# Kernel tuning notes

Measured on AMD Instinct MI355X. Metric: run time of the kernel, lower is better.

Reference implementation:

```python
import jax, jax.numpy as jnp
import numpy as np

N, M, D = 32768, 4096, 128  # samples, SOM units (64x64), input_dim
GRID_H, GRID_W = 64, 64


def setup_inputs() -> dict:
    key = jax.random.key(0)
    k1, k2 = jax.random.split(key)
    inputs = jax.random.normal(k1, (N, D), dtype=jnp.float32)
    # SOM2D.__init__: weights = torch.rand(size, input_dim)
    weights = jax.random.uniform(k2, (M, D), dtype=jnp.float32)
    # grid = meshgrid(arange(H), arange(W)) -> [M, 2] integer unit coordinates
    gx, gy = jnp.meshgrid(jnp.arange(GRID_H), jnp.arange(GRID_W), indexing='ij')
    grid = jnp.stack([gx, gy], axis=-1).reshape(-1, 2).astype(jnp.int32)
    return {"inputs": inputs, "weights": weights, "grid": grid}


def reference(inputs, weights, grid):
    # sed(x, y): squared Euclidean distance [N, M].
    # tensor the torch code materializes; same math.
    x_sq = jnp.sum(inputs * inputs, axis=1, keepdims=True)        # [N, 1]
    w_sq = jnp.sum(weights * weights, axis=1)                      # [M]
    cross = jnp.einsum('nd,md->nm', inputs, weights)               # [N, M]
    distances = x_sq + w_sq - 2.0 * cross                          # [N, M]
    # wtac: argmin over units, then lookup grid coordinates of the winner.
    winning_indices = jnp.argmin(distances, axis=1)                # [N]
    winning_labels = grid[winning_indices]                         # [N, 2]
    return winning_labels
```

## Files before the change

### kernel.cpp

```cpp
#include <hip/hip_runtime.h>
#include <float.h>
#include <stdint.h>


constexpr int D = 128;

typedef _Float16 f16x8 __attribute__((ext_vector_type(8)));
typedef float    f32x4 __attribute__((ext_vector_type(4)));

__device__ __forceinline__ void cvt_split(const float4& a0, const float4& a1,
                                          f16x8& h, f16x8& l) {
    float v[8] = {a0.x, a0.y, a0.z, a0.w, a1.x, a1.y, a1.z, a1.w};
#pragma unroll
    for (int j = 0; j < 8; ++j) {
        _Float16 hh = (_Float16)v[j];
        h[j] = hh;
        l[j] = (_Float16)(v[j] - (float)hh);
    }
}

__global__ __launch_bounds__(256) void prep_kernel(
        const float* __restrict__ w, f16x8* __restrict__ hG,
        f16x8* __restrict__ lG, float* __restrict__ wsq, int M) {
    int g = blockIdx.x * 256 + threadIdx.x;
    if (g >= M * 16) return;
    int u = g >> 4, o = g & 15;
    const float4* wp = reinterpret_cast<const float4*>(w + (size_t)u * D + o * 8);
    float4 a0 = wp[0], a1 = wp[1];
    f16x8 h, l;
    cvt_split(a0, a1, h, l);
    float ss = 0.f;
    ss = fmaf(a0.x, a0.x, ss); ss = fmaf(a0.y, a0.y, ss);
    ss = fmaf(a0.z, a0.z, ss); ss = fmaf(a0.w, a0.w, ss);
    ss = fmaf(a1.x, a1.x, ss); ss = fmaf(a1.y, a1.y, ss);
    ss = fmaf(a1.z, a1.z, ss); ss = fmaf(a1.w, a1.w, ss);
#pragma unroll
    for (int m = 1; m < 16; m <<= 1) ss += __shfl_xor(ss, m, 64);
    if (o == 0) wsq[u] = ss;
    int slot = ((u >> 5) << 9) + ((o >> 2) << 7) + (((u >> 4) & 1) << 6)
             + ((o & 3) << 4) + (u & 15);
    hG[slot] = h;
    lG[slot] = l;
}

__global__ void finalize(const unsigned long long* __restrict__ keys,
                         const int* __restrict__ grid, int* __restrict__ out,
                         int N, int UG) {
    int s = blockIdx.x * blockDim.x + threadIdx.x;
    if (s >= N) return;
    unsigned long long k = keys[s];
    for (int g = 1; g < UG; ++g) {
        unsigned long long kg = keys[(size_t)g * N + s];
        if (kg < k) k = kg;
    }
    int idx = (int)(unsigned)(k & 0xFFFFFFFFull);
    out[2 * s]     = grid[2 * idx];
    out[2 * s + 1] = grid[2 * idx + 1];
}

template <bool PARTIAL>
__global__ __launch_bounds__(256, 2) void som_main(
        const float* __restrict__ x, const f16x8* __restrict__ hG,
        const f16x8* __restrict__ lG, const float* __restrict__ wsq,
        const int* __restrict__ grid, int* __restrict__ out,
        unsigned long long* __restrict__ keys,
        int unitGroups, int M, int N) {
    __shared__ f16x8 albuf[4 * 1024];

    const int tid  = threadIdx.x;
    const int lane = tid & 63;
    const int wv   = tid >> 6;
    const int c    = lane & 15;
    const int q    = lane >> 4;

    const int ug    = blockIdx.x % unitGroups;
    const int sg    = blockIdx.x / unitGroups;
    const int sWave = sg * 256 + wv * 64;

    f16x8* myAl = &albuf[wv * 1024];

    f16x8 Ah[16];
#pragma unroll
    for (int i = 0; i < 4; ++i) {
        const float* xr = x + (size_t)(sWave + 16 * i + c) * D + q * 8;
#pragma unroll
        for (int s = 0; s < 4; ++s) {
            float4 a0 = *reinterpret_cast<const float4*>(xr + 32 * s);
            float4 a1 = *reinterpret_cast<const float4*>(xr + 32 * s + 4);
            f16x8 h, l;
            cvt_split(a0, a1, h, l);
            Ah[i * 4 + s] = h;
            myAl[(i * 4 + s) * 64 + lane] = l;
        }
    }

    float bestD[16];
    int   bestI[16];
#pragma unroll
    for (int sl = 0; sl < 16; ++sl) { bestD[sl] = FLT_MAX; bestI[sl] = 0; }

    const int tilesPer = (M / 32) / unitGroups;
    const int tile0    = ug * tilesPer;

    for (int tt = 0; tt < tilesPer; ++tt) {
        const int tile = tile0 + tt;
        const f16x8* hp = hG + ((size_t)tile << 9) + lane;
        const f16x8* lp = lG + ((size_t)tile << 9) + lane;

        f16x8 bh[8], bl[8];
#pragma unroll
        for (int s = 0; s < 4; ++s)
#pragma unroll
            for (int t = 0; t < 2; ++t)
                bh[s * 2 + t] = hp[s * 128 + t * 64];
#pragma unroll
        for (int s = 0; s < 4; ++s)
#pragma unroll
            for (int t = 0; t < 2; ++t)
                bl[s * 2 + t] = lp[s * 128 + t * 64];

        const int uTile = tile * 32;
        const float wq0 = wsq[uTile + c];
        const float wq1 = wsq[uTile + 16 + c];

        f32x4 acc[8];
#pragma unroll
        for (int f = 0; f < 8; ++f) acc[f] = (f32x4){0.f, 0.f, 0.f, 0.f};

#pragma unroll
        for (int s = 0; s < 4; ++s)
#pragma unroll
            for (int i = 0; i < 4; ++i)
#pragma unroll
                for (int t = 0; t < 2; ++t)
                    acc[i * 2 + t] = __builtin_amdgcn_mfma_f32_16x16x32_f16(
                        Ah[i * 4 + s], bh[s * 2 + t], acc[i * 2 + t], 0, 0, 0);
#pragma unroll
        for (int s = 0; s < 4; ++s) {
            f16x8 al[4];
#pragma unroll
            for (int i = 0; i < 4; ++i) al[i] = myAl[(i * 4 + s) * 64 + lane];
#pragma unroll
            for (int i = 0; i < 4; ++i)
#pragma unroll
                for (int t = 0; t < 2; ++t)
                    acc[i * 2 + t] = __builtin_amdgcn_mfma_f32_16x16x32_f16(
                        al[i], bh[s * 2 + t], acc[i * 2 + t], 0, 0, 0);
        }
#pragma unroll
        for (int s = 0; s < 4; ++s)
#pragma unroll
            for (int i = 0; i < 4; ++i)
#pragma unroll
                for (int t = 0; t < 2; ++t)
                    acc[i * 2 + t] = __builtin_amdgcn_mfma_f32_16x16x32_f16(
                        Ah[i * 4 + s], bl[s * 2 + t], acc[i * 2 + t], 0, 0, 0);

#pragma unroll
        for (int t = 0; t < 2; ++t) {
            const int n    = uTile + 16 * t + c;
            const float wq = t == 0 ? wq0 : wq1;
#pragma unroll
            for (int i = 0; i < 4; ++i) {
                f32x4 a = acc[i * 2 + t];
#pragma unroll
                for (int r = 0; r < 4; ++r) {
                    float score = fmaf(-2.f, a[r], wq);
                    int sl = i * 4 + r;
                    if (score < bestD[sl]) { bestD[sl] = score; bestI[sl] = n; }
                }
            }
        }
    }

#pragma unroll
    for (int sl = 0; sl < 16; ++sl) {
        float d   = bestD[sl];
        int   idx = bestI[sl];
#pragma unroll
        for (int m = 1; m < 16; m <<= 1) {
            float od = __shfl_xor(d, m, 64);
            int   oi = __shfl_xor(idx, m, 64);
            if (od < d || (od == d && oi < idx)) { d = od; idx = oi; }
        }
        if (c == 0) {
            const int sOut = sWave + 16 * (sl >> 2) + 4 * q + (sl & 3);
            if (PARTIAL) {
                unsigned ub = __float_as_uint(d);
                ub = (ub & 0x80000000u) ? ~ub : (ub | 0x80000000u);
                unsigned long long key = ((unsigned long long)ub << 32) | (unsigned)idx;
                keys[(size_t)ug * N + sOut] = key;
            } else {
                out[2 * sOut]     = grid[2 * idx];
                out[2 * sOut + 1] = grid[2 * idx + 1];
            }
        }
    }
}

extern "C" void kernel_launch(void* const* d_in, const int* in_sizes, int n_in,
                              void* d_out, int out_size, void* d_ws, size_t ws_size,
                              hipStream_t stream) {
    const float* x    = (const float*)d_in[0];
    const float* w    = (const float*)d_in[1];
    const int*   grid = (const int*)d_in[2];
    int* out = (int*)d_out;

    const int N = in_sizes[0] / D;
    const int M = in_sizes[1] / D;

    const size_t hlBytes   = (size_t)M * D * 2;
    const size_t baseBytes = 2 * hlBytes + (size_t)M * 4;

    f16x8* hG  = (f16x8*)d_ws;
    f16x8* lG  = (f16x8*)((char*)d_ws + hlBytes);
    float* wsq = (float*)((char*)d_ws + 2 * hlBytes);
    unsigned long long* keys = (unsigned long long*)((char*)d_ws + baseBytes);

    prep_kernel<<<(M * 16 + 255) / 256, 256, 0, stream>>>(w, hG, lG, wsq, M);

    const int sampleGroups = N / 256;
    int UG = 0;
    if (ws_size >= baseBytes + 4ull * N * 8) UG = 4;
    else if (ws_size >= baseBytes + 2ull * N * 8) UG = 2;

    if (UG > 0) {
        som_main<true><<<sampleGroups * UG, 256, 0, stream>>>(
            x, hG, lG, wsq, grid, out, keys, UG, M, N);
        finalize<<<(N + 255) / 256, 256, 0, stream>>>(keys, grid, out, N, UG);
    } else {
        som_main<false><<<sampleGroups, 256, 0, stream>>>(
            x, hG, lG, wsq, grid, out, nullptr, 1, M, N);
    }
}
```

Baseline: 156.3 us.

## Merge split-K reduction into main kernel with atomicMin and raise occupancy

```diff
diff --git a/kernel.cpp b/kernel.cpp
--- a/kernel.cpp
+++ b/kernel.cpp
@@ -21,8 +21,12 @@
 
 __global__ __launch_bounds__(256) void prep_kernel(
         const float* __restrict__ w, f16x8* __restrict__ hG,
-        f16x8* __restrict__ lG, float* __restrict__ wsq, int M) {
+        f16x8* __restrict__ lG, float* __restrict__ wsq, int M,
+        unsigned long long* __restrict__ keys, unsigned* __restrict__ cnt,
+        int N, int nGroups) {
     int g = blockIdx.x * 256 + threadIdx.x;
+    if (keys && g < N) keys[g] = ~0ull;
+    if (cnt && g < nGroups) cnt[g] = 0u;
     if (g >= M * 16) return;
     int u = g >> 4, o = g & 15;
     const float4* wp = reinterpret_cast<const float4*>(w + (size_t)u * D + o * 8);
@@ -43,29 +47,15 @@
     lG[slot] = l;
 }
 
-__global__ void finalize(const unsigned long long* __restrict__ keys,
-                         const int* __restrict__ grid, int* __restrict__ out,
-                         int N, int UG) {
-    int s = blockIdx.x * blockDim.x + threadIdx.x;
-    if (s >= N) return;
-    unsigned long long k = keys[s];
-    for (int g = 1; g < UG; ++g) {
-        unsigned long long kg = keys[(size_t)g * N + s];
-        if (kg < k) k = kg;
-    }
-    int idx = (int)(unsigned)(k & 0xFFFFFFFFull);
-    out[2 * s]     = grid[2 * idx];
-    out[2 * s + 1] = grid[2 * idx + 1];
-}
-
 template <bool PARTIAL>
-__global__ __launch_bounds__(256, 2) void som_main(
+__global__ __launch_bounds__(256, 3) void som_main(
         const float* __restrict__ x, const f16x8* __restrict__ hG,
         const f16x8* __restrict__ lG, const float* __restrict__ wsq,
         const int* __restrict__ grid, int* __restrict__ out,
-        unsigned long long* __restrict__ keys,
-        int unitGroups, int M, int N) {
-    __shared__ f16x8 albuf[4 * 1024];
+        unsigned long long* __restrict__ keys, unsigned* __restrict__ cnt,
+        int unitGroups, int tilesQ, int tilesR, int N) {
+    __shared__ f16x8 albuf[4 * 768];
+    __shared__ int lastFlag;
 
     const int tid  = threadIdx.x;
     const int lane = tid & 63;
@@ -77,9 +67,10 @@
     const int sg    = blockIdx.x / unitGroups;
     const int sWave = sg * 256 + wv * 64;
 
-    f16x8* myAl = &albuf[wv * 1024];
+    f16x8* myAl = &albuf[wv * 768];
 
     f16x8 Ah[16];
+    f16x8 Al3[4];
 #pragma unroll
     for (int i = 0; i < 4; ++i) {
         const float* xr = x + (size_t)(sWave + 16 * i + c) * D + q * 8;
@@ -90,7 +81,8 @@
             f16x8 h, l;
             cvt_split(a0, a1, h, l);
             Ah[i * 4 + s] = h;
-            myAl[(i * 4 + s) * 64 + lane] = l;
+            if (s < 3) myAl[(i * 3 + s) * 64 + lane] = l;
+            else       Al3[i] = l;
         }
     }
 
@@ -99,10 +91,10 @@
 #pragma unroll
     for (int sl = 0; sl < 16; ++sl) { bestD[sl] = FLT_MAX; bestI[sl] = 0; }
 
-    const int tilesPer = (M / 32) / unitGroups;
-    const int tile0    = ug * tilesPer;
-
-    for (int tt = 0; tt < tilesPer; ++tt) {
+    const int tile0  = ug * tilesQ + (ug < tilesR ? ug : tilesR);
+    const int tcount = tilesQ + (ug < tilesR ? 1 : 0);
+
+    for (int tt = 0; tt < tcount; ++tt) {
         const int tile = tile0 + tt;
         const f16x8* hp = hG + ((size_t)tile << 9) + lane;
         const f16x8* lp = lG + ((size_t)tile << 9) + lane;
@@ -127,6 +119,7 @@
 #pragma unroll
         for (int f = 0; f < 8; ++f) acc[f] = (f32x4){0.f, 0.f, 0.f, 0.f};
 
+        __builtin_amdgcn_s_setprio(1);
 #pragma unroll
         for (int s = 0; s < 4; ++s)
 #pragma unroll
@@ -139,7 +132,8 @@
         for (int s = 0; s < 4; ++s) {
             f16x8 al[4];
 #pragma unroll
-            for (int i = 0; i < 4; ++i) al[i] = myAl[(i * 4 + s) * 64 + lane];
+            for (int i = 0; i < 4; ++i)
+                al[i] = (s < 3) ? myAl[(i * 3 + s) * 64 + lane] : Al3[i];
 #pragma unroll
             for (int i = 0; i < 4; ++i)
 #pragma unroll
@@ -155,6 +149,7 @@
                 for (int t = 0; t < 2; ++t)
                     acc[i * 2 + t] = __builtin_amdgcn_mfma_f32_16x16x32_f16(
                         Ah[i * 4 + s], bl[s * 2 + t], acc[i * 2 + t], 0, 0, 0);
+        __builtin_amdgcn_s_setprio(0);
 
 #pragma unroll
         for (int t = 0; t < 2; ++t) {
@@ -189,11 +184,26 @@
                 unsigned ub = __float_as_uint(d);
                 ub = (ub & 0x80000000u) ? ~ub : (ub | 0x80000000u);
                 unsigned long long key = ((unsigned long long)ub << 32) | (unsigned)idx;
-                keys[(size_t)ug * N + sOut] = key;
+                atomicMin(&keys[sOut], key);
             } else {
                 out[2 * sOut]     = grid[2 * idx];
                 out[2 * sOut + 1] = grid[2 * idx + 1];
             }
+        }
+    }
+
+    if (PARTIAL) {
+        __threadfence();
+        __syncthreads();
+        if (tid == 0)
+            lastFlag = (atomicAdd(&cnt[sg], 1u) == (unsigned)(unitGroups - 1));
+        __syncthreads();
+        if (lastFlag) {
+            const int s0 = sg * 256 + tid;
+            unsigned long long k = atomicMin(&keys[s0], ~0ull);
+            int idx = (int)(unsigned)(k & 0xFFFFFFFFull);
+            out[2 * s0]     = grid[2 * idx];
+            out[2 * s0 + 1] = grid[2 * idx + 1];
         }
     }
 }
@@ -211,25 +221,28 @@
 
     const size_t hlBytes   = (size_t)M * D * 2;
     const size_t baseBytes = 2 * hlBytes + (size_t)M * 4;
+    const int sampleGroups = N / 256;
+    const size_t needBytes = baseBytes + (size_t)N * 8 + (size_t)sampleGroups * 4;
 
     f16x8* hG  = (f16x8*)d_ws;
     f16x8* lG  = (f16x8*)((char*)d_ws + hlBytes);
     float* wsq = (float*)((char*)d_ws + 2 * hlBytes);
     unsigned long long* keys = (unsigned long long*)((char*)d_ws + baseBytes);
-
-    prep_kernel<<<(M * 16 + 255) / 256, 256, 0, stream>>>(w, hG, lG, wsq, M);
-
-    const int sampleGroups = N / 256;
-    int UG = 0;
-    if (ws_size >= baseBytes + 4ull * N * 8) UG = 4;
-    else if (ws_size >= baseBytes + 2ull * N * 8) UG = 2;
-
-    if (UG > 0) {
+    unsigned* cnt = (unsigned*)((char*)d_ws + baseBytes + (size_t)N * 8);
+
+    const int tiles = M / 32;
+    const int UG = (ws_size >= needBytes) ? 6 : 1;
+
+    prep_kernel<<<(M * 16 + 255) / 256, 256, 0, stream>>>(
+        w, hG, lG, wsq, M,
+        UG > 1 ? keys : nullptr, UG > 1 ? cnt : nullptr, N, sampleGroups);
+
+    const int tq = tiles / UG, trm = tiles % UG;
+    if (UG > 1) {
         som_main<true><<<sampleGroups * UG, 256, 0, stream>>>(
-            x, hG, lG, wsq, grid, out, keys, UG, M, N);
-        finalize<<<(N + 255) / 256, 256, 0, stream>>>(keys, grid, out, N, UG);
+            x, hG, lG, wsq, grid, out, keys, cnt, UG, tq, trm, N);
     } else {
         som_main<false><<<sampleGroups, 256, 0, stream>>>(
-            x, hG, lG, wsq, grid, out, nullptr, 1, M, N);
-    }
-}
+            x, hG, lG, wsq, grid, out, nullptr, nullptr, 1, tiles, 0, N);
+    }
+}
```

Result: slower. 528.2 us (+237.9%).

## Screen winners with hi-only fp16 pass and recompute ambiguous samples exactly

Applied to the files above, without the earlier changes.

```diff
diff --git a/kernel.cpp b/kernel.cpp
--- a/kernel.cpp
+++ b/kernel.cpp
@@ -19,9 +19,25 @@
     }
 }
 
+__device__ __forceinline__ unsigned monoU(float f) {
+    unsigned u = __float_as_uint(f);
+    return (u & 0x80000000u) ? ~u : (u | 0x80000000u);
+}
+__device__ __forceinline__ float monoF(unsigned t) {
+    unsigned b = (t & 0x80000000u) ? (t ^ 0x80000000u) : ~t;
+    return __uint_as_float(b);
+}
+
+__global__ void init_kernel(unsigned* scal, unsigned* cnt, int nGroups) {
+    int t = threadIdx.x;
+    if (t < 4) scal[t] = 0u;
+    for (int i = t; i < nGroups; i += 256) cnt[i] = 0u;
+}
+
 __global__ __launch_bounds__(256) void prep_kernel(
         const float* __restrict__ w, f16x8* __restrict__ hG,
-        f16x8* __restrict__ lG, float* __restrict__ wsq, int M) {
+        f16x8* __restrict__ lG, float* __restrict__ wsq, int M,
+        unsigned* __restrict__ scal) {
     int g = blockIdx.x * 256 + threadIdx.x;
     if (g >= M * 16) return;
     int u = g >> 4, o = g & 15;
@@ -29,60 +45,66 @@
     float4 a0 = wp[0], a1 = wp[1];
     f16x8 h, l;
     cvt_split(a0, a1, h, l);
-    float ss = 0.f;
+    float ss = 0.f, hs = 0.f, ls = 0.f;
     ss = fmaf(a0.x, a0.x, ss); ss = fmaf(a0.y, a0.y, ss);
     ss = fmaf(a0.z, a0.z, ss); ss = fmaf(a0.w, a0.w, ss);
     ss = fmaf(a1.x, a1.x, ss); ss = fmaf(a1.y, a1.y, ss);
     ss = fmaf(a1.z, a1.z, ss); ss = fmaf(a1.w, a1.w, ss);
 #pragma unroll
-    for (int m = 1; m < 16; m <<= 1) ss += __shfl_xor(ss, m, 64);
+    for (int j = 0; j < 8; ++j) {
+        float hf = (float)h[j], lf = (float)l[j];
+        hs = fmaf(hf, hf, hs);
+        ls = fmaf(lf, lf, ls);
+    }
+#pragma unroll
+    for (int m = 1; m < 16; m <<= 1) {
+        ss += __shfl_xor(ss, m, 64);
+        hs += __shfl_xor(hs, m, 64);
+        ls += __shfl_xor(ls, m, 64);
+    }
     if (o == 0) wsq[u] = ss;
+    if (scal) {
+        float hm = hs, lm = ls;
+        hm = fmaxf(hm, __shfl_xor(hm, 16, 64)); hm = fmaxf(hm, __shfl_xor(hm, 32, 64));
+        lm = fmaxf(lm, __shfl_xor(lm, 16, 64)); lm = fmaxf(lm, __shfl_xor(lm, 32, 64));
+        if ((threadIdx.x & 63) == 0) {
+            atomicMax(&scal[0], __float_as_uint(hm));
+            atomicMax(&scal[1], __float_as_uint(lm));
+        }
+    }
     int slot = ((u >> 5) << 9) + ((o >> 2) << 7) + (((u >> 4) & 1) << 6)
              + ((o & 3) << 4) + (u & 15);
     hG[slot] = h;
     lG[slot] = l;
 }
 
-__global__ void finalize(const unsigned long long* __restrict__ keys,
-                         const int* __restrict__ grid, int* __restrict__ out,
-                         int N, int UG) {
-    int s = blockIdx.x * blockDim.x + threadIdx.x;
-    if (s >= N) return;
-    unsigned long long k = keys[s];
-    for (int g = 1; g < UG; ++g) {
-        unsigned long long kg = keys[(size_t)g * N + s];
-        if (kg < k) k = kg;
-    }
-    int idx = (int)(unsigned)(k & 0xFFFFFFFFull);
-    out[2 * s]     = grid[2 * idx];
-    out[2 * s + 1] = grid[2 * idx + 1];
-}
-
-template <bool PARTIAL>
-__global__ __launch_bounds__(256, 2) void som_main(
+template <int UGT>
+__global__ __launch_bounds__(256, 2) void som_hi(
         const float* __restrict__ x, const f16x8* __restrict__ hG,
-        const f16x8* __restrict__ lG, const float* __restrict__ wsq,
-        const int* __restrict__ grid, int* __restrict__ out,
-        unsigned long long* __restrict__ keys,
-        int unitGroups, int M, int N) {
-    __shared__ f16x8 albuf[4 * 1024];
-
+        const float* __restrict__ wsq, const int* __restrict__ grid,
+        int* __restrict__ out, const unsigned* __restrict__ scal,
+        unsigned long long* __restrict__ b1key, unsigned* __restrict__ b2u,
+        float* __restrict__ thrS, unsigned* __restrict__ cnt,
+        unsigned* __restrict__ flagCnt, int* __restrict__ flagList,
+        int tilesPer, int N) {
     const int tid  = threadIdx.x;
     const int lane = tid & 63;
     const int wv   = tid >> 6;
     const int c    = lane & 15;
     const int q    = lane >> 4;
 
-    const int ug    = blockIdx.x % unitGroups;
-    const int sg    = blockIdx.x / unitGroups;
+    const int ug    = blockIdx.x % UGT;
+    const int sg    = blockIdx.x / UGT;
     const int sWave = sg * 256 + wv * 64;
 
-    f16x8* myAl = &albuf[wv * 1024];
+    const float maxWH = sqrtf(__uint_as_float(scal[0]));
+    const float maxWL = sqrtf(__uint_as_float(scal[1]));
 
     f16x8 Ah[16];
 #pragma unroll
     for (int i = 0; i < 4; ++i) {
         const float* xr = x + (size_t)(sWave + 16 * i + c) * D + q * 8;
+        float xh2 = 0.f, xl2 = 0.f;
 #pragma unroll
         for (int s = 0; s < 4; ++s) {
             float4 a0 = *reinterpret_cast<const float4*>(xr + 32 * s);
@@ -90,34 +112,35 @@
             f16x8 h, l;
             cvt_split(a0, a1, h, l);
             Ah[i * 4 + s] = h;
-            myAl[(i * 4 + s) * 64 + lane] = l;
-        }
-    }
-
-    float bestD[16];
-    int   bestI[16];
-#pragma unroll
-    for (int sl = 0; sl < 16; ++sl) { bestD[sl] = FLT_MAX; bestI[sl] = 0; }
-
-    const int tilesPer = (M / 32) / unitGroups;
-    const int tile0    = ug * tilesPer;
-
+#pragma unroll
+            for (int j = 0; j < 8; ++j) {
+                float hf = (float)h[j], lf = (float)l[j];
+                xh2 = fmaf(hf, hf, xh2);
+                xl2 = fmaf(lf, lf, xl2);
+            }
+        }
+        xh2 += __shfl_xor(xh2, 16, 64); xh2 += __shfl_xor(xh2, 32, 64);
+        xl2 += __shfl_xor(xl2, 16, 64); xl2 += __shfl_xor(xl2, 32, 64);
+        if (q == 0)
+            thrS[sWave + 16 * i + c] =
+                4.0f * (sqrtf(xl2) * (maxWH + maxWL) + sqrtf(xh2) * maxWL) + 0.04f;
+    }
+
+    float b1d[16]; int b1i[16]; float b2d[16];
+#pragma unroll
+    for (int sl = 0; sl < 16; ++sl) { b1d[sl] = FLT_MAX; b1i[sl] = 0; b2d[sl] = FLT_MAX; }
+
+    const int tile0 = ug * tilesPer;
     for (int tt = 0; tt < tilesPer; ++tt) {
         const int tile = tile0 + tt;
         const f16x8* hp = hG + ((size_t)tile << 9) + lane;
-        const f16x8* lp = lG + ((size_t)tile << 9) + lane;
-
-        f16x8 bh[8], bl[8];
+
+        f16x8 bh[8];
 #pragma unroll
         for (int s = 0; s < 4; ++s)
 #pragma unroll
             for (int t = 0; t < 2; ++t)
                 bh[s * 2 + t] = hp[s * 128 + t * 64];
-#pragma unroll
-        for (int s = 0; s < 4; ++s)
-#pragma unroll
-            for (int t = 0; t < 2; ++t)
-                bl[s * 2 + t] = lp[s * 128 + t * 64];
 
         const int uTile = tile * 32;
         const float wq0 = wsq[uTile + c];
@@ -135,26 +158,6 @@
                 for (int t = 0; t < 2; ++t)
                     acc[i * 2 + t] = __builtin_amdgcn_mfma_f32_16x16x32_f16(
                         Ah[i * 4 + s], bh[s * 2 + t], acc[i * 2 + t], 0, 0, 0);
-#pragma unroll
-        for (int s = 0; s < 4; ++s) {
-            f16x8 al[4];
-#pragma unroll
-            for (int i = 0; i < 4; ++i) al[i] = myAl[(i * 4 + s) * 64 + lane];
-#pragma unroll
-            for (int i = 0; i < 4; ++i)
-#pragma unroll
-                for (int t = 0; t < 2; ++t)
-                    acc[i * 2 + t] = __builtin_amdgcn_mfma_f32_16x16x32_f16(
-                        al[i], bh[s * 2 + t], acc[i * 2 + t], 0, 0, 0);
-        }
-#pragma unroll
-        for (int s = 0; s < 4; ++s)
-#pragma unroll
-            for (int i = 0; i < 4; ++i)
-#pragma unroll
-                for (int t = 0; t < 2; ++t)
-                    acc[i * 2 + t] = __builtin_amdgcn_mfma_f32_16x16x32_f16(
-                        Ah[i * 4 + s], bl[s * 2 + t], acc[i * 2 + t], 0, 0, 0);
 
 #pragma unroll
         for (int t = 0; t < 2; ++t) {
@@ -165,9 +168,10 @@
                 f32x4 a = acc[i * 2 + t];
 #pragma unroll
                 for (int r = 0; r < 4; ++r) {
-                    float score = fmaf(-2.f, a[r], wq);
+                    float v = fmaf(-2.f, a[r], wq);
                     int sl = i * 4 + r;
-                    if (score < bestD[sl]) { bestD[sl] = score; bestI[sl] = n; }
+                    if (v < b1d[sl]) { b2d[sl] = b1d[sl]; b1d[sl] = v; b1i[sl] = n; }
+                    else if (v < b2d[sl]) b2d[sl] = v;
                 }
             }
         }
@@ -175,24 +179,189 @@
 
 #pragma unroll
     for (int sl = 0; sl < 16; ++sl) {
-        float d   = bestD[sl];
-        int   idx = bestI[sl];
+        float d1 = b1d[sl]; int i1 = b1i[sl]; float d2 = b2d[sl];
 #pragma unroll
         for (int m = 1; m < 16; m <<= 1) {
-            float od = __shfl_xor(d, m, 64);
-            int   oi = __shfl_xor(idx, m, 64);
-            if (od < d || (od == d && oi < idx)) { d = od; idx = oi; }
+            float od1 = __shfl_xor(d1, m, 64);
+            int   oi1 = __shfl_xor(i1, m, 64);
+            float od2 = __shfl_xor(d2, m, 64);
+            float nd2 = fminf(fminf(d2, od2), fmaxf(d1, od1));
+            bool take = od1 < d1 || (od1 == d1 && oi1 < i1);
+            d1 = take ? od1 : d1;
+            i1 = take ? oi1 : i1;
+            d2 = nd2;
         }
         if (c == 0) {
             const int sOut = sWave + 16 * (sl >> 2) + 4 * q + (sl & 3);
-            if (PARTIAL) {
-                unsigned ub = __float_as_uint(d);
-                ub = (ub & 0x80000000u) ? ~ub : (ub | 0x80000000u);
-                unsigned long long key = ((unsigned long long)ub << 32) | (unsigned)idx;
-                keys[(size_t)ug * N + sOut] = key;
+            unsigned long long k = ((unsigned long long)monoU(d1) << 32) | (unsigned)i1;
+            atomicExch(&b1key[(size_t)ug * N + sOut], k);
+            atomicExch(&b2u[(size_t)ug * N + sOut], monoU(d2));
+        }
+    }
+
+    __threadfence();
+    int old = 0;
+    if (lane == 0) old = (int)atomicAdd(&cnt[sg], 1u);
+    old = __shfl(old, 0, 64);
+    if (old == 4 * UGT - 1) {
+        __threadfence();
+#pragma unroll
+        for (int j = 0; j < 4; ++j) {
+            const int s = sg * 256 + j * 64 + lane;
+            unsigned long long k[UGT]; unsigned u2[UGT];
+#pragma unroll
+            for (int g2 = 0; g2 < UGT; ++g2) {
+                k[g2]  = atomicMin(&b1key[(size_t)g2 * N + s], ~0ull);
+                u2[g2] = atomicMin(&b2u[(size_t)g2 * N + s], 0xFFFFFFFFu);
+            }
+            unsigned long long g1 = k[0];
+#pragma unroll
+            for (int g2 = 1; g2 < UGT; ++g2) if (k[g2] < g1) g1 = k[g2];
+            unsigned gb2 = 0xFFFFFFFFu;
+#pragma unroll
+            for (int g2 = 0; g2 < UGT; ++g2) {
+                unsigned hi = (unsigned)(k[g2] >> 32);
+                if (k[g2] != g1 && hi < gb2) gb2 = hi;
+                if (u2[g2] < gb2) gb2 = u2[g2];
+            }
+            float d1 = monoF((unsigned)(g1 >> 32));
+            float d2 = monoF(gb2);
+            if (d2 - d1 > thrS[s]) {
+                int idx = (int)(unsigned)(g1 & 0xFFFFFFFFull);
+                out[2 * s]     = grid[2 * idx];
+                out[2 * s + 1] = grid[2 * idx + 1];
             } else {
-                out[2 * sOut]     = grid[2 * idx];
-                out[2 * sOut + 1] = grid[2 * idx + 1];
+                unsigned pos = atomicAdd(flagCnt, 1u);
+                flagList[pos] = s;
+            }
+        }
+    }
+}
+
+template <bool GATHER>
+__global__ __launch_bounds__(256, 2) void som_fix(
+        const float* __restrict__ x, const f16x8* __restrict__ hG,
+        const f16x8* __restrict__ lG, const float* __restrict__ wsq,
+        const int* __restrict__ grid, int* __restrict__ out,
+        const int* __restrict__ flagList, const unsigned* __restrict__ totalPtr,
+        int totalN, int tiles) {
+    __shared__ f16x8 albuf[4 * 1024];
+
+    const int tid  = threadIdx.x;
+    const int lane = tid & 63;
+    const int wv   = tid >> 6;
+    const int c    = lane & 15;
+    const int q    = lane >> 4;
+
+    const int total = GATHER ? (int)totalPtr[0] : totalN;
+    f16x8* myAl = &albuf[wv * 1024];
+
+    for (int base = blockIdx.x * 256; base < total; base += gridDim.x * 256) {
+        const int sBase = base + wv * 64;
+
+        f16x8 Ah[16];
+#pragma unroll
+        for (int i = 0; i < 4; ++i) {
+            int p = sBase + 16 * i + c;
+            int s = GATHER ? flagList[p < total ? p : total - 1] : p;
+            const float* xr = x + (size_t)s * D + q * 8;
+#pragma unroll
+            for (int ks = 0; ks < 4; ++ks) {
+                float4 a0 = *reinterpret_cast<const float4*>(xr + 32 * ks);
+                float4 a1 = *reinterpret_cast<const float4*>(xr + 32 * ks + 4);
+                f16x8 h, l;
+                cvt_split(a0, a1, h, l);
+                Ah[i * 4 + ks] = h;
+                myAl[(i * 4 + ks) * 64 + lane] = l;
+            }
+        }
+
+        float bestD[16]; int bestI[16];
+#pragma unroll
+        for (int sl = 0; sl < 16; ++sl) { bestD[sl] = FLT_MAX; bestI[sl] = 0; }
+
+        for (int tile = 0; tile < tiles; ++tile) {
+            const f16x8* hp = hG + ((size_t)tile << 9) + lane;
+            const f16x8* lp = lG + ((size_t)tile << 9) + lane;
+
+            f16x8 bh[8], bl[8];
+#pragma unroll
+            for (int s = 0; s < 4; ++s)
+#pragma unroll
+                for (int t = 0; t < 2; ++t) {
+                    bh[s * 2 + t] = hp[s * 128 + t * 64];
+                    bl[s * 2 + t] = lp[s * 128 + t * 64];
+                }
+
+            const int uTile = tile * 32;
+            const float wq0 = wsq[uTile + c];
+            const float wq1 = wsq[uTile + 16 + c];
+
+            f32x4 acc[8];
+#pragma unroll
+            for (int f = 0; f < 8; ++f) acc[f] = (f32x4){0.f, 0.f, 0.f, 0.f};
+
+#pragma unroll
+            for (int s = 0; s < 4; ++s)
+#pragma unroll
+                for (int i = 0; i < 4; ++i)
+#pragma unroll
+                    for (int t = 0; t < 2; ++t)
+                        acc[i * 2 + t] = __builtin_amdgcn_mfma_f32_16x16x32_f16(
+                            Ah[i * 4 + s], bh[s * 2 + t], acc[i * 2 + t], 0, 0, 0);
+#pragma unroll
+            for (int s = 0; s < 4; ++s) {
+                f16x8 al[4];
+#pragma unroll
+                for (int i = 0; i < 4; ++i) al[i] = myAl[(i * 4 + s) * 64 + lane];
+#pragma unroll
+                for (int i = 0; i < 4; ++i)
+#pragma unroll
+                    for (int t = 0; t < 2; ++t)
+                        acc[i * 2 + t] = __builtin_amdgcn_mfma_f32_16x16x32_f16(
+                            al[i], bh[s * 2 + t], acc[i * 2 + t], 0, 0, 0);
+            }
+#pragma unroll
+            for (int s = 0; s < 4; ++s)
+#pragma unroll
+                for (int i = 0; i < 4; ++i)
+#pragma unroll
+                    for (int t = 0; t < 2; ++t)
+                        acc[i * 2 + t] = __builtin_amdgcn_mfma_f32_16x16x32_f16(
+                            Ah[i * 4 + s], bl[s * 2 + t], acc[i * 2 + t], 0, 0, 0);
+
+#pragma unroll
+            for (int t = 0; t < 2; ++t) {
+                const int n    = uTile + 16 * t + c;
+                const float wq = t == 0 ? wq0 : wq1;
+#pragma unroll
+                for (int i = 0; i < 4; ++i) {
+                    f32x4 a = acc[i * 2 + t];
+#pragma unroll
+                    for (int r = 0; r < 4; ++r) {
+                        float score = fmaf(-2.f, a[r], wq);
+                        int sl = i * 4 + r;
+                        if (score < bestD[sl]) { bestD[sl] = score; bestI[sl] = n; }
+                    }
+                }
+            }
+        }
+
+#pragma unroll
+        for (int sl = 0; sl < 16; ++sl) {
+            float d   = bestD[sl];
+            int   idx = bestI[sl];
+#pragma unroll
+            for (int m = 1; m < 16; m <<= 1) {
+                float od = __shfl_xor(d, m, 64);
+                int   oi = __shfl_xor(idx, m, 64);
+                if (od < d || (od == d && oi < idx)) { d = od; idx = oi; }
+            }
+            if (c == 0) {
+                int p2 = sBase + 16 * (sl >> 2) + 4 * q + (sl & 3);
+                int s2 = GATHER ? flagList[p2 < total ? p2 : total - 1] : p2;
+                out[2 * s2]     = grid[2 * idx];
+                out[2 * s2 + 1] = grid[2 * idx + 1];
             }
         }
     }
@@ -208,28 +377,41 @@
 
     const int N = in_sizes[0] / D;
     const int M = in_sizes[1] / D;
-
-    const size_t hlBytes   = (size_t)M * D * 2;
-    const size_t baseBytes = 2 * hlBytes + (size_t)M * 4;
+    const int UG      = 4;
+    const int tiles   = M / 32;
+    const int nGroups = N / 256;
+
+    const size_t hlB    = (size_t)M * D * 2;
+    const size_t oWsq   = 2 * hlB;
+    const size_t oScal  = oWsq + (size_t)M * 4;
+    const size_t oCnt   = oScal + 32;
+    const size_t oThr   = oCnt + (size_t)nGroups * 4;
+    const size_t oB1    = oThr + (size_t)N * 4;
+    const size_t oB2    = oB1 + (size_t)UG * N * 8;
+    const size_t oFlag  = oB2 + (size_t)UG * N * 4;
+    const size_t need   = oFlag + (size_t)N * 4;
 
     f16x8* hG  = (f16x8*)d_ws;
-    f16x8* lG  = (f16x8*)((char*)d_ws + hlBytes);
-    float* wsq = (float*)((char*)d_ws + 2 * hlBytes);
-    unsigned long long* keys = (unsigned long long*)((char*)d_ws + baseBytes);
-
-    prep_kernel<<<(M * 16 + 255) / 256, 256, 0, stream>>>(w, hG, lG, wsq, M);
-
-    const int sampleGroups = N / 256;
-    int UG = 0;
-    if (ws_size >= baseBytes + 4ull * N * 8) UG = 4;
-    else if (ws_size >= baseBytes + 2ull * N * 8) UG = 2;
-
-    if (UG > 0) {
-        som_main<true><<<sampleGroups * UG, 256, 0, stream>>>(
-            x, hG, lG, wsq, grid, out, keys, UG, M, N);
-        finalize<<<(N + 255) / 256, 256, 0, stream>>>(keys, grid, out, N, UG);
+    f16x8* lG  = (f16x8*)((char*)d_ws + hlB);
+    float* wsq = (float*)((char*)d_ws + oWsq);
+    unsigned* scal = (unsigned*)((char*)d_ws + oScal);
+    unsigned* cnt  = (unsigned*)((char*)d_ws + oCnt);
+    float* thrS    = (float*)((char*)d_ws + oThr);
+    unsigned long long* b1key = (unsigned long long*)((char*)d_ws + oB1);
+    unsigned* b2u  = (unsigned*)((char*)d_ws + oB2);
+    int* flagList  = (int*)((char*)d_ws + oFlag);
+
+    if (ws_size >= need) {
+        init_kernel<<<1, 256, 0, stream>>>(scal, cnt, nGroups);
+        prep_kernel<<<(M * 16 + 255) / 256, 256, 0, stream>>>(w, hG, lG, wsq, M, scal);
+        som_hi<4><<<nGroups * UG, 256, 0, stream>>>(
+            x, hG, wsq, grid, out, scal, b1key, b2u, thrS, cnt,
+            &scal[2], flagList, tiles / UG, N);
+        som_fix<true><<<128, 256, 0, stream>>>(
+            x, hG, lG, wsq, grid, out, flagList, &scal[2], 0, tiles);
     } else {
-        som_main<false><<<sampleGroups, 256, 0, stream>>>(
-            x, hG, lG, wsq, grid, out, nullptr, 1, M, N);
-    }
-}
+        prep_kernel<<<(M * 16 + 255) / 256, 256, 0, stream>>>(w, hG, lG, wsq, M, nullptr);
+        som_fix<false><<<N / 256, 256, 0, stream>>>(
+            x, hG, lG, wsq, grid, out, nullptr, nullptr, N, tiles);
+    }
+}
```

Result: slower. 497.8 us (+218.4%).
